# Kernel tuning notes

Measured on AMD Instinct MI355X. Metric: run time of the kernel, lower is better.

The kernel has to match this reference:

```python
import jax, jax.numpy as jnp
import numpy as np

N_NODES = 50000
N_EDGES = 600000
DIMS = [1280, 512, 300, 300]


def setup_inputs() -> dict:
    key = jax.random.key(0)
    ks = jax.random.split(key, 8)
    x = jax.random.normal(ks[0], (N_NODES, DIMS[0]), dtype=jnp.float32)
    edge_index = jax.random.randint(ks[1], (2, N_EDGES), 0, N_NODES, dtype=jnp.int64)
    def w(k, i, o):
        return jax.random.normal(k, (i, o), dtype=jnp.float32) * (1.0 / np.sqrt(i))
    W1 = w(ks[2], DIMS[0], DIMS[1]); b1 = jnp.zeros((DIMS[1],), jnp.float32)
    W2 = w(ks[3], DIMS[1], DIMS[2]); b2 = jnp.zeros((DIMS[2],), jnp.float32)
    W3 = w(ks[4], DIMS[2], DIMS[3]); b3 = jnp.zeros((DIMS[3],), jnp.float32)
    return {"x": x, "W1": W1, "b1": b1, "W2": W2, "b2": b2,
            "W3": W3, "b3": b3, "edge_index": edge_index}


def gcn_conv(x, W, b, src, dst, n):
    """PyG GCNConv: add self-loops, symmetric D^-1/2 (A+I) D^-1/2 aggregation."""
    h = x @ W  # [N, out]
    loops = jnp.arange(n, dtype=src.dtype)
    s = jnp.concatenate([src, loops])  # [E+N]
    d = jnp.concatenate([dst, loops])
    deg = jax.ops.segment_sum(jnp.ones_like(d, dtype=h.dtype), d, num_segments=n)
    dinv = jnp.where(deg > 0, jax.lax.rsqrt(deg), 0.0)
    norm = dinv[s] * dinv[d]  # [E+N]
    out = jax.ops.segment_sum(h[s] * norm[:, None], d, num_segments=n)
    return out + b


def reference(x, W1, b1, W2, b2, W3, b3, edge_index):
    src, dst = edge_index[0], edge_index[1]
    n = x.shape[0]
    # dropout is identity in eval mode; pertubed=False path
    h = jax.nn.relu(gcn_conv(x, W1, b1, src, dst, n))
    h = jax.nn.relu(gcn_conv(h, W2, b2, src, dst, n))
    h = jax.nn.relu(gcn_conv(h, W3, b3, src, dst, n))
    return h  # [N, 300]; per-graph split is a trivial mask over data.batch
```

## Files before the change

kernel.cpp:

```cpp
#include <hip/hip_runtime.h>

typedef _Float16 f16;
typedef _Float16 f16x2 __attribute__((ext_vector_type(2)));
typedef _Float16 f16x4 __attribute__((ext_vector_type(4)));
typedef _Float16 f16x8 __attribute__((ext_vector_type(8)));
typedef float f32x4 __attribute__((ext_vector_type(4)));

#define N_NODES 50000
#define N_EDGES 600000

__device__ __forceinline__ void gl_lds16(const void* g, void* l) {
  __builtin_amdgcn_global_load_lds(
      (__attribute__((address_space(1))) void*)(g),
      (__attribute__((address_space(3))) void*)(l), 16, 0, 0);
}

__global__ void k_setup(const float* __restrict__ x, f16* __restrict__ xh,
                        const float* __restrict__ W1, f16* __restrict__ w1h,
                        const float* __restrict__ W2, f16* __restrict__ w2h,
                        const float* __restrict__ W3, f16* __restrict__ w3h,
                        const float* __restrict__ b2, float* __restrict__ bp2,
                        const float* __restrict__ b3, float* __restrict__ bp3,
                        const int* __restrict__ edst, int* __restrict__ deg) {
  const int b = blockIdx.x, t = threadIdx.x;
  if (b < 62500) {
    long i = (long)b * 256 + t;
    float4 v = ((const float4*)x)[i];
    f16x4 o;
    o[0] = (f16)v.x; o[1] = (f16)v.y; o[2] = (f16)v.z; o[3] = (f16)v.w;
    ((f16x4*)xh)[i] = o;
  } else if (b < 64844) {
    int e = (b - 62500) * 256 + t;
    if (e < N_EDGES) atomicAdd(&deg[edst[e]], 1);
  } else if (b < 67404) {
    int idx = (b - 64844) * 256 + t;
    int n = idx / 1280, k = idx - n * 1280;
    w1h[idx] = (f16)W1[(size_t)k * 512 + n];
  } else if (b < 68004) {
    int bb = b - 67404;
    int n = bb >> 1, k = (bb & 1) * 256 + t;
    if (k < 512) w2h[(size_t)n * 512 + k] = (f16)W2[(size_t)k * 300 + n];
  } else if (b < 68604) {
    int bb = b - 68004;
    int n = bb >> 1, k = (bb & 1) * 256 + t;
    if (k < 320) w3h[(size_t)n * 320 + k] = (k < 300) ? (f16)W3[(size_t)k * 300 + n] : (f16)0.f;
  } else if (b < 68606) {
    int i = (b - 68604) * 256 + t;
    if (i < 320) bp2[i] = (i < 300) ? b2[i] : 0.f;
  } else {
    int i = (b - 68606) * 256 + t;
    if (i < 320) bp3[i] = (i < 300) ? b3[i] : 0.f;
  }
}

__device__ __forceinline__ int block_incl_scan256(int v, int t) {
  __shared__ int wsum[4];
  const int lane = t & 63, w = t >> 6;
  int incl = v;
#pragma unroll
  for (int off = 1; off < 64; off <<= 1) {
    int u = __shfl_up(incl, off, 64);
    if (lane >= off) incl += u;
  }
  if (lane == 63) wsum[w] = incl;
  __syncthreads();
  int add = 0;
#pragma unroll
  for (int k = 0; k < 4; ++k)
    if (k < w) add += wsum[k];
  return incl + add;
}

__global__ void k_scan1(const int* __restrict__ deg, float* __restrict__ dinv,
                        int* __restrict__ bsum, int n) {
  __shared__ int ws4[4];
  const int t = threadIdx.x, b = blockIdx.x;
  const int i = b * 256 + t;
  int v = (i < n) ? deg[i] : 0;
  if (i < n) dinv[i] = rsqrtf((float)(v + 1));
  int s = v;
#pragma unroll
  for (int off = 1; off < 64; off <<= 1) s += __shfl_xor(s, off, 64);
  if ((t & 63) == 0) ws4[t >> 6] = s;
  __syncthreads();
  if (t == 0) bsum[b] = ws4[0] + ws4[1] + ws4[2] + ws4[3];
}

__global__ void k_scan2(const int* __restrict__ bsum, int* __restrict__ bpre,
                        int* __restrict__ rowptr, int nb, int n) {
  const int t = threadIdx.x;
  int v = (t < nb) ? bsum[t] : 0;
  int incl = block_incl_scan256(v, t);
  if (t < nb) bpre[t] = incl - v;
  if (t == 255) rowptr[n] = incl;
}

__global__ void k_scan3(const int* __restrict__ deg, const int* __restrict__ bpre,
                        int* __restrict__ rowptr, int* __restrict__ rptr2, int n) {
  const int t = threadIdx.x, b = blockIdx.x;
  const int i = b * 256 + t;
  int v = (i < n) ? deg[i] : 0;
  int incl = block_incl_scan256(v, t);
  int ex = bpre[b] + incl - v;
  if (i < n) { rowptr[i] = ex; rptr2[i] = ex; }
}

__global__ void k_fill(const int* __restrict__ src, const int* __restrict__ dst,
                       int* __restrict__ rptr2, int2* __restrict__ meta,
                       const float* __restrict__ dinv, int E) {
  int e = blockIdx.x * 256 + threadIdx.x;
  if (e < E) {
    int d = dst[e], s = src[e];
    int pos = atomicAdd(&rptr2[d], 1);
    float w = dinv[s] * dinv[d];
    meta[pos] = make_int2(s, __float_as_int(w));
  }
}

__global__ __launch_bounds__(256, 3)
void gemm_f16_tn(const f16* __restrict__ A, const f16* __restrict__ B,
                 f16* __restrict__ C, int M, int N, int K,
                 int lda, int ldb, int ldc) {
  __shared__ __align__(16) f16 As[2][128 * 32];
  __shared__ __align__(16) f16 Bs[2][128 * 32];
  const int tid = threadIdx.x;
  const int wave = tid >> 6;
  const int lane = tid & 63;
  const int bm = blockIdx.y, bn = blockIdx.x;

  const int srow = tid >> 2;
  const int sunit = (tid & 3) ^ ((tid >> 3) & 3);
  long ar0 = (long)bm * 128 + srow;      if (ar0 > M - 1) ar0 = M - 1;
  long ar1 = (long)bm * 128 + srow + 64; if (ar1 > M - 1) ar1 = M - 1;
  long br0 = (long)bn * 128 + srow;      if (br0 > N - 1) br0 = N - 1;
  long br1 = (long)bn * 128 + srow + 64; if (br1 > N - 1) br1 = N - 1;
  const char* aSrc0 = (const char*)(A + ar0 * lda) + sunit * 16;
  const char* aSrc1 = (const char*)(A + ar1 * lda) + sunit * 16;
  const char* bSrc0 = (const char*)(B + br0 * ldb) + sunit * 16;
  const char* bSrc1 = (const char*)(B + br1 * ldb) + sunit * 16;

  const int r16 = lane & 15;
  const int kq = lane >> 4;
  const int wm = wave & 1, wn = wave >> 1;

  int aoff[4], boff[4];
#pragma unroll
  for (int t = 0; t < 4; ++t) {
    int arow = wm * 64 + t * 16 + r16;
    aoff[t] = arow * 64 + ((kq ^ ((arow >> 1) & 3)) << 4);
    int brow = wn * 64 + t * 16 + r16;
    boff[t] = brow * 64 + ((kq ^ ((brow >> 1) & 3)) << 4);
  }

  f32x4 acc[4][4] = {};

  gl_lds16(aSrc0, (char*)As + wave * 1024);
  gl_lds16(aSrc1, (char*)As + 4096 + wave * 1024);
  gl_lds16(bSrc0, (char*)Bs + wave * 1024);
  gl_lds16(bSrc1, (char*)Bs + 4096 + wave * 1024);
  __syncthreads();

  int buf = 0;
  for (int k0 = 0; k0 < K; k0 += 32) {
    if (k0 + 32 < K) {
      const size_t kb = (size_t)(k0 + 32) * 2;
      const int nb = buf ^ 1;
      gl_lds16(aSrc0 + kb, (char*)As + nb * 8192 + wave * 1024);
      gl_lds16(aSrc1 + kb, (char*)As + nb * 8192 + 4096 + wave * 1024);
      gl_lds16(bSrc0 + kb, (char*)Bs + nb * 8192 + wave * 1024);
      gl_lds16(bSrc1 + kb, (char*)Bs + nb * 8192 + 4096 + wave * 1024);
    }

    const char* baseA = (const char*)As + buf * 8192;
    const char* baseB = (const char*)Bs + buf * 8192;
    f16x8 af[4], bf[4];
#pragma unroll
    for (int t = 0; t < 4; ++t) {
      af[t] = *(const f16x8*)(baseA + aoff[t]);
      bf[t] = *(const f16x8*)(baseB + boff[t]);
    }
#pragma unroll
    for (int mt = 0; mt < 4; ++mt)
#pragma unroll
      for (int nt = 0; nt < 4; ++nt)
        acc[mt][nt] = __builtin_amdgcn_mfma_f32_16x16x32_f16(af[mt], bf[nt], acc[mt][nt], 0, 0, 0);

    __syncthreads();
    buf ^= 1;
  }

  const int crow0 = bm * 128 + wm * 64;
  const int ccol0 = bn * 128 + wn * 64;
#pragma unroll
  for (int mt = 0; mt < 4; ++mt)
#pragma unroll
    for (int nt = 0; nt < 4; ++nt)
#pragma unroll
      for (int r = 0; r < 4; ++r) {
        int row = crow0 + mt * 16 + kq * 4 + r;
        int col = ccol0 + nt * 16 + r16;
        if (row < M && col < ldc)
          C[(size_t)row * ldc + col] = (col < N) ? (f16)acc[mt][nt][r] : (f16)0.f;
      }
}

template <int LDH, int ACT, bool F16OUT, int DOUT>
__global__ __launch_bounds__(256, 8)
void agg_relu3(const f16* __restrict__ h, const int* __restrict__ rowptr,
               const int2* __restrict__ meta, const float* __restrict__ dinv,
               const float* __restrict__ bias, void* __restrict__ outp, int nNodes) {
  const int tid = threadIdx.x;
  const int lane = tid & 63;
  const int node = blockIdx.x * 4 + (tid >> 6);
  if (node >= nNodes) return;
  const int r0 = __builtin_amdgcn_readfirstlane(rowptr[node]);
  const int r1 = __builtin_amdgcn_readfirstlane(rowptr[node + 1]);
  const float dv = __builtin_bit_cast(
      float, __builtin_amdgcn_readfirstlane(__builtin_bit_cast(int, dinv[node])));

  const int hoff = (lane < ACT ? lane : ACT - 1) * 8;
  const f16* hp = h + hoff;

  float acc[8];
  {
    f16x8 v = *(const f16x8*)(hp + (size_t)node * LDH);
    const float w0 = dv * dv;
#pragma unroll
    for (int j = 0; j < 8; ++j) acc[j] = w0 * (float)v[j];
  }

  for (int base = r0; base < r1; base += 64) {
    const int idx = base + lane;
    int2 m = (idx < r1) ? meta[idx] : make_int2(0, 0);
    const int cnt = min(64, r1 - base);
    int j = 0;
    for (; j + 2 <= cnt; j += 2) {
      int s0 = __shfl(m.x, j, 64);
      int s1 = __shfl(m.x, j + 1, 64);
      float w0 = __int_as_float(__shfl(m.y, j, 64));
      float w1 = __int_as_float(__shfl(m.y, j + 1, 64));
      f16x8 v0 = *(const f16x8*)(hp + (size_t)s0 * LDH);
      f16x8 v1 = *(const f16x8*)(hp + (size_t)s1 * LDH);
#pragma unroll
      for (int q = 0; q < 8; ++q) acc[q] = fmaf(w0, (float)v0[q], acc[q]);
#pragma unroll
      for (int q = 0; q < 8; ++q) acc[q] = fmaf(w1, (float)v1[q], acc[q]);
    }
    if (j < cnt) {
      int s0 = __shfl(m.x, j, 64);
      float w0 = __int_as_float(__shfl(m.y, j, 64));
      f16x8 v0 = *(const f16x8*)(hp + (size_t)s0 * LDH);
#pragma unroll
      for (int q = 0; q < 8; ++q) acc[q] = fmaf(w0, (float)v0[q], acc[q]);
    }
  }

  float4 bv0 = *(const float4*)(bias + hoff);
  float4 bv1 = *(const float4*)(bias + hoff + 4);
  float o[8];
  o[0] = fmaxf(acc[0] + bv0.x, 0.f); o[1] = fmaxf(acc[1] + bv0.y, 0.f);
  o[2] = fmaxf(acc[2] + bv0.z, 0.f); o[3] = fmaxf(acc[3] + bv0.w, 0.f);
  o[4] = fmaxf(acc[4] + bv1.x, 0.f); o[5] = fmaxf(acc[5] + bv1.y, 0.f);
  o[6] = fmaxf(acc[6] + bv1.z, 0.f); o[7] = fmaxf(acc[7] + bv1.w, 0.f);

  if constexpr (F16OUT) {
    if (lane < ACT) {
      f16x8 ov;
#pragma unroll
      for (int j = 0; j < 8; ++j) ov[j] = (f16)o[j];
      *(f16x8*)((f16*)outp + (size_t)node * LDH + lane * 8) = ov;
    }
  } else {
    float* orow = (float*)outp + (size_t)node * DOUT + lane * 8;
    if (lane * 8 + 4 <= DOUT)
      *(float4*)(orow) = make_float4(o[0], o[1], o[2], o[3]);
    if (lane * 8 + 8 <= DOUT)
      *(float4*)(orow + 4) = make_float4(o[4], o[5], o[6], o[7]);
  }
}

extern "C" void kernel_launch(void* const* d_in, const int* in_sizes, int n_in,
                              void* d_out, int out_size, void* d_ws, size_t ws_size,
                              hipStream_t stream) {
  const float* x  = (const float*)d_in[0];
  const float* W1 = (const float*)d_in[1];
  const float* b1 = (const float*)d_in[2];
  const float* W2 = (const float*)d_in[3];
  const float* b2 = (const float*)d_in[4];
  const float* W3 = (const float*)d_in[5];
  const float* b3 = (const float*)d_in[6];
  const int* eidx = (const int*)d_in[7];
  const int* esrc = eidx;
  const int* edst = eidx + N_EDGES;
  float* out = (float*)d_out;

  char* ws = (char*)d_ws;
  f16* xh = (f16*)(ws);
  f16* h2 = (f16*)(ws);
  f16* g2 = (f16*)(ws + 32000000);
  f16* h3 = (f16*)(ws + 64000000);
  f16* h1 = (f16*)(ws + 128000000);
  f16* g1 = (f16*)(ws + 179200000);
  f16* w1h = (f16*)(ws + 230400000);
  f16* w2h = (f16*)(ws + 231710720);
  f16* w3h = (f16*)(ws + 232017920);
  float* bp2 = (float*)(ws + 232209920);
  float* bp3 = (float*)(ws + 232211200);
  int* deg    = (int*)(ws + 232212480);
  float* dinv = (float*)(ws + 232412480);
  int* rowptr = (int*)(ws + 232612480);
  int* rptr2  = (int*)(ws + 232812484);
  int* bsum   = (int*)(ws + 233012488);
  int* bpre   = (int*)(ws + 233013288);
  int2* meta  = (int2*)(ws + 233014088);

  hipMemsetAsync(deg, 0, N_NODES * sizeof(int), stream);

  k_setup<<<68608, 256, 0, stream>>>(x, xh, W1, w1h, W2, w2h, W3, w3h,
                                     b2, bp2, b3, bp3, edst, deg);

  k_scan1<<<196, 256, 0, stream>>>(deg, dinv, bsum, N_NODES);
  k_scan2<<<1, 256, 0, stream>>>(bsum, bpre, rowptr, 196, N_NODES);
  k_scan3<<<196, 256, 0, stream>>>(deg, bpre, rowptr, rptr2, N_NODES);
  k_fill<<<2344, 256, 0, stream>>>(esrc, edst, rptr2, meta, dinv, N_EDGES);

  gemm_f16_tn<<<dim3(4, 391), 256, 0, stream>>>(xh, w1h, h1, N_NODES, 512, 1280, 1280, 1280, 512);
  agg_relu3<512, 64, true, 0><<<12500, 256, 0, stream>>>(h1, rowptr, meta, dinv, b1, g1, N_NODES);

  gemm_f16_tn<<<dim3(3, 391), 256, 0, stream>>>(g1, w2h, h2, N_NODES, 300, 512, 512, 512, 320);
  agg_relu3<320, 40, true, 0><<<12500, 256, 0, stream>>>(h2, rowptr, meta, dinv, bp2, g2, N_NODES);

  gemm_f16_tn<<<dim3(3, 391), 256, 0, stream>>>(g2, w3h, h3, N_NODES, 300, 320, 320, 320, 320);
  agg_relu3<320, 38, false, 300><<<12500, 256, 0, stream>>>(h3, rowptr, meta, dinv, bp3, out, N_NODES);
}
```

Measured before the change: 815.3 us.

## Triple-buffer GEMM LDS tiles with one barrier per k-step

Changes the f16 GEMM from double to triple buffering of the A and B shared-memory tiles. It prefetches two k-steps ahead and uses a partial vmcnt wait plus a single raw barrier per iteration instead of two __syncthreads. The aim is more overlap between global-to-LDS loads and MFMA work and less barrier stall. LDS use per block grows from 32 KB to 48 KB, which may lower occupancy against the 3-blocks launch bound. The code also assumes K is at least 64 and a multiple of 32.

```diff
diff --git a/kernel.cpp b/kernel.cpp
--- a/kernel.cpp
+++ b/kernel.cpp
@@ -121,8 +121,8 @@
 void gemm_f16_tn(const f16* __restrict__ A, const f16* __restrict__ B,
                  f16* __restrict__ C, int M, int N, int K,
                  int lda, int ldb, int ldc) {
-  __shared__ __align__(16) f16 As[2][128 * 32];
-  __shared__ __align__(16) f16 Bs[2][128 * 32];
+  __shared__ __align__(16) f16 As[3][128 * 32];
+  __shared__ __align__(16) f16 Bs[3][128 * 32];
   const int tid = threadIdx.x;
   const int wave = tid >> 6;
   const int lane = tid & 63;
@@ -138,6 +138,8 @@
   const char* aSrc1 = (const char*)(A + ar1 * lda) + sunit * 16;
   const char* bSrc0 = (const char*)(B + br0 * ldb) + sunit * 16;
   const char* bSrc1 = (const char*)(B + br1 * ldb) + sunit * 16;
+  char* const ldsA = (char*)As + wave * 1024;
+  char* const ldsB = (char*)Bs + wave * 1024;
 
   const int r16 = lane & 15;
   const int kq = lane >> 4;
@@ -153,40 +155,70 @@
   }
 
   f32x4 acc[4][4] = {};
-
-  gl_lds16(aSrc0, (char*)As + wave * 1024);
-  gl_lds16(aSrc1, (char*)As + 4096 + wave * 1024);
-  gl_lds16(bSrc0, (char*)Bs + wave * 1024);
-  gl_lds16(bSrc1, (char*)Bs + 4096 + wave * 1024);
-  __syncthreads();
+  const int nt = K >> 5;
+
+  gl_lds16(aSrc0, ldsA);
+  gl_lds16(aSrc1, ldsA + 4096);
+  gl_lds16(bSrc0, ldsB);
+  gl_lds16(bSrc1, ldsB + 4096);
+  gl_lds16(aSrc0 + 64, ldsA + 8192);
+  gl_lds16(aSrc1 + 64, ldsA + 8192 + 4096);
+  gl_lds16(bSrc0 + 64, ldsB + 8192);
+  gl_lds16(bSrc1 + 64, ldsB + 8192 + 4096);
 
   int buf = 0;
-  for (int k0 = 0; k0 < K; k0 += 32) {
-    if (k0 + 32 < K) {
-      const size_t kb = (size_t)(k0 + 32) * 2;
-      const int nb = buf ^ 1;
-      gl_lds16(aSrc0 + kb, (char*)As + nb * 8192 + wave * 1024);
-      gl_lds16(aSrc1 + kb, (char*)As + nb * 8192 + 4096 + wave * 1024);
-      gl_lds16(bSrc0 + kb, (char*)Bs + nb * 8192 + wave * 1024);
-      gl_lds16(bSrc1 + kb, (char*)Bs + nb * 8192 + 4096 + wave * 1024);
+  for (int t = 0; t < nt - 1; ++t) {
+    asm volatile("s_waitcnt vmcnt(4)" ::: "memory");
+    __builtin_amdgcn_sched_barrier(0);
+    __builtin_amdgcn_s_barrier();
+    __builtin_amdgcn_sched_barrier(0);
+
+    if (t + 2 < nt) {
+      const size_t kb = (size_t)(t + 2) * 64;
+      int nbuf = buf + 2; if (nbuf >= 3) nbuf -= 3;
+      char* dA = (char*)As + nbuf * 8192 + wave * 1024;
+      char* dB = (char*)Bs + nbuf * 8192 + wave * 1024;
+      gl_lds16(aSrc0 + kb, dA);
+      gl_lds16(aSrc1 + kb, dA + 4096);
+      gl_lds16(bSrc0 + kb, dB);
+      gl_lds16(bSrc1 + kb, dB + 4096);
     }
 
     const char* baseA = (const char*)As + buf * 8192;
     const char* baseB = (const char*)Bs + buf * 8192;
     f16x8 af[4], bf[4];
 #pragma unroll
-    for (int t = 0; t < 4; ++t) {
-      af[t] = *(const f16x8*)(baseA + aoff[t]);
-      bf[t] = *(const f16x8*)(baseB + boff[t]);
+    for (int q = 0; q < 4; ++q) {
+      af[q] = *(const f16x8*)(baseA + aoff[q]);
+      bf[q] = *(const f16x8*)(baseB + boff[q]);
     }
 #pragma unroll
     for (int mt = 0; mt < 4; ++mt)
 #pragma unroll
-      for (int nt = 0; nt < 4; ++nt)
-        acc[mt][nt] = __builtin_amdgcn_mfma_f32_16x16x32_f16(af[mt], bf[nt], acc[mt][nt], 0, 0, 0);
-
-    __syncthreads();
-    buf ^= 1;
+      for (int nt2 = 0; nt2 < 4; ++nt2)
+        acc[mt][nt2] = __builtin_amdgcn_mfma_f32_16x16x32_f16(af[mt], bf[nt2], acc[mt][nt2], 0, 0, 0);
+
+    buf = (buf + 1 == 3) ? 0 : buf + 1;
+  }
+
+  asm volatile("s_waitcnt vmcnt(0)" ::: "memory");
+  __builtin_amdgcn_sched_barrier(0);
+  __builtin_amdgcn_s_barrier();
+  __builtin_amdgcn_sched_barrier(0);
+  {
+    const char* baseA = (const char*)As + buf * 8192;
+    const char* baseB = (const char*)Bs + buf * 8192;
+    f16x8 af[4], bf[4];
+#pragma unroll
+    for (int q = 0; q < 4; ++q) {
+      af[q] = *(const f16x8*)(baseA + aoff[q]);
+      bf[q] = *(const f16x8*)(baseB + boff[q]);
+    }
+#pragma unroll
+    for (int mt = 0; mt < 4; ++mt)
+#pragma unroll
+      for (int nt2 = 0; nt2 < 4; ++nt2)
+        acc[mt][nt2] = __builtin_amdgcn_mfma_f32_16x16x32_f16(af[mt], bf[nt2], acc[mt][nt2], 0, 0, 0);
   }
 
   const int crow0 = bm * 128 + wm * 64;
@@ -194,13 +226,13 @@
 #pragma unroll
   for (int mt = 0; mt < 4; ++mt)
 #pragma unroll
-    for (int nt = 0; nt < 4; ++nt)
+    for (int nt2 = 0; nt2 < 4; ++nt2)
 #pragma unroll
       for (int r = 0; r < 4; ++r) {
         int row = crow0 + mt * 16 + kq * 4 + r;
-        int col = ccol0 + nt * 16 + r16;
+        int col = ccol0 + nt2 * 16 + r16;
         if (row < M && col < ldc)
-          C[(size_t)row * ldc + col] = (col < N) ? (f16)acc[mt][nt][r] : (f16)0.f;
+          C[(size_t)row * ldc + col] = (col < N) ? (f16)acc[mt][nt2][r] : (f16)0.f;
       }
 }
 
```

New measurement: 819.5 us. Within noise of the previous version (+0.5%).

## Use single-buffered BK=64 GEMM tiles with 8-way XOR LDS swizzle

Applied to the files above, without the earlier changes.

The f16 GEMM now loads 64-wide K slices into a single LDS buffer per operand instead of double-buffered 32-wide slices, using an 8-unit XOR swizzle and per-wave row ownership for the global-to-LDS copies. Each iteration issues two MFMA sub-steps per barrier pair, halving the number of loop iterations and barrier overhead. The trade-off is that loads are no longer overlapped with compute through double buffering, so each iteration waits for its own loads. K must be a multiple of 64, which holds for 1280/512 but depends on padding for 300.

```diff
diff --git a/kernel.cpp b/kernel.cpp
--- a/kernel.cpp
+++ b/kernel.cpp
@@ -121,72 +121,67 @@
 void gemm_f16_tn(const f16* __restrict__ A, const f16* __restrict__ B,
                  f16* __restrict__ C, int M, int N, int K,
                  int lda, int ldb, int ldc) {
-  __shared__ __align__(16) f16 As[2][128 * 32];
-  __shared__ __align__(16) f16 Bs[2][128 * 32];
+  __shared__ __align__(16) f16 As[128 * 64];
+  __shared__ __align__(16) f16 Bs[128 * 64];
   const int tid = threadIdx.x;
   const int wave = tid >> 6;
   const int lane = tid & 63;
   const int bm = blockIdx.y, bn = blockIdx.x;
 
-  const int srow = tid >> 2;
-  const int sunit = (tid & 3) ^ ((tid >> 3) & 3);
-  long ar0 = (long)bm * 128 + srow;      if (ar0 > M - 1) ar0 = M - 1;
-  long ar1 = (long)bm * 128 + srow + 64; if (ar1 > M - 1) ar1 = M - 1;
-  long br0 = (long)bn * 128 + srow;      if (br0 > N - 1) br0 = N - 1;
-  long br1 = (long)bn * 128 + srow + 64; if (br1 > N - 1) br1 = N - 1;
-  const char* aSrc0 = (const char*)(A + ar0 * lda) + sunit * 16;
-  const char* aSrc1 = (const char*)(A + ar1 * lda) + sunit * 16;
-  const char* bSrc0 = (const char*)(B + br0 * ldb) + sunit * 16;
-  const char* bSrc1 = (const char*)(B + br1 * ldb) + sunit * 16;
+  const int r8 = lane >> 3;
+  const int sunit = (lane & 7) ^ r8;
+  const char* aSrc[4];
+  const char* bSrc[4];
+#pragma unroll
+  for (int c = 0; c < 4; ++c) {
+    long ar = (long)bm * 128 + wave * 32 + c * 8 + r8; if (ar > M - 1) ar = M - 1;
+    long br = (long)bn * 128 + wave * 32 + c * 8 + r8; if (br > N - 1) br = N - 1;
+    aSrc[c] = (const char*)(A + ar * lda) + sunit * 16;
+    bSrc[c] = (const char*)(B + br * ldb) + sunit * 16;
+  }
 
   const int r16 = lane & 15;
   const int kq = lane >> 4;
   const int wm = wave & 1, wn = wave >> 1;
 
-  int aoff[4], boff[4];
+  int aoff[4][2], boff[4][2];
 #pragma unroll
   for (int t = 0; t < 4; ++t) {
-    int arow = wm * 64 + t * 16 + r16;
-    aoff[t] = arow * 64 + ((kq ^ ((arow >> 1) & 3)) << 4);
-    int brow = wn * 64 + t * 16 + r16;
-    boff[t] = brow * 64 + ((kq ^ ((brow >> 1) & 3)) << 4);
+#pragma unroll
+    for (int ks = 0; ks < 2; ++ks) {
+      int arow = wm * 64 + t * 16 + r16;
+      aoff[t][ks] = arow * 128 + ((((ks << 2) + kq) ^ (arow & 7)) << 4);
+      int brow = wn * 64 + t * 16 + r16;
+      boff[t][ks] = brow * 128 + ((((ks << 2) + kq) ^ (brow & 7)) << 4);
+    }
   }
 
   f32x4 acc[4][4] = {};
 
-  gl_lds16(aSrc0, (char*)As + wave * 1024);
-  gl_lds16(aSrc1, (char*)As + 4096 + wave * 1024);
-  gl_lds16(bSrc0, (char*)Bs + wave * 1024);
-  gl_lds16(bSrc1, (char*)Bs + 4096 + wave * 1024);
-  __syncthreads();
-
-  int buf = 0;
-  for (int k0 = 0; k0 < K; k0 += 32) {
-    if (k0 + 32 < K) {
-      const size_t kb = (size_t)(k0 + 32) * 2;
-      const int nb = buf ^ 1;
-      gl_lds16(aSrc0 + kb, (char*)As + nb * 8192 + wave * 1024);
-      gl_lds16(aSrc1 + kb, (char*)As + nb * 8192 + 4096 + wave * 1024);
-      gl_lds16(bSrc0 + kb, (char*)Bs + nb * 8192 + wave * 1024);
-      gl_lds16(bSrc1 + kb, (char*)Bs + nb * 8192 + 4096 + wave * 1024);
-    }
-
-    const char* baseA = (const char*)As + buf * 8192;
-    const char* baseB = (const char*)Bs + buf * 8192;
-    f16x8 af[4], bf[4];
-#pragma unroll
-    for (int t = 0; t < 4; ++t) {
-      af[t] = *(const f16x8*)(baseA + aoff[t]);
-      bf[t] = *(const f16x8*)(baseB + boff[t]);
-    }
-#pragma unroll
-    for (int mt = 0; mt < 4; ++mt)
-#pragma unroll
-      for (int nt = 0; nt < 4; ++nt)
-        acc[mt][nt] = __builtin_amdgcn_mfma_f32_16x16x32_f16(af[mt], bf[nt], acc[mt][nt], 0, 0, 0);
-
+  for (int k0 = 0; k0 < K; k0 += 64) {
     __syncthreads();
-    buf ^= 1;
+    const size_t kb = (size_t)k0 * 2;
+#pragma unroll
+    for (int c = 0; c < 4; ++c) {
+      gl_lds16(aSrc[c] + kb, (char*)As + (wave * 32 + c * 8) * 128);
+      gl_lds16(bSrc[c] + kb, (char*)Bs + (wave * 32 + c * 8) * 128);
+    }
+    __syncthreads();
+
+#pragma unroll
+    for (int ks = 0; ks < 2; ++ks) {
+      f16x8 af[4], bf[4];
+#pragma unroll
+      for (int t = 0; t < 4; ++t) {
+        af[t] = *(const f16x8*)((const char*)As + aoff[t][ks]);
+        bf[t] = *(const f16x8*)((const char*)Bs + boff[t][ks]);
+      }
+#pragma unroll
+      for (int mt = 0; mt < 4; ++mt)
+#pragma unroll
+        for (int nt = 0; nt < 4; ++nt)
+          acc[mt][nt] = __builtin_amdgcn_mfma_f32_16x16x32_f16(af[mt], bf[nt], acc[mt][nt], 0, 0, 0);
+    }
   }
 
   const int crow0 = bm * 128 + wm * 64;
```

New measurement: 795.4 us. 2.4% less time.
